# Kernel tuning notes

Measured on AMD Instinct MI355X. Metric: run time of the kernel, lower is better.

Reference implementation:

```python
import jax, jax.numpy as jnp
import numpy as np

B, C, H, W = 32, 4, 512, 512
T = 64  # Angular_representive_Threshold
GROUPS = 2


def setup_inputs() -> dict:
    key = jax.random.key(0)
    k1, k2 = jax.random.split(key)
    x_real = jax.random.normal(k1, (B, C, H, W), dtype=jnp.float32)
    x_imag = jax.random.normal(k2, (B, C, H, W), dtype=jnp.float32)
    return {"x_real": x_real, "x_imag": x_imag}


def reference(x_real, x_imag):
    # Complex angular-delay input, split into 2 groups of 2 channels (torch.chunk dim=1)
    x = (x_real + 1j * x_imag).astype(jnp.complex64)            # [B,4,H,W]
    xg = x.reshape(B, GROUPS, 2, H, W)                          # [B,g,ch,H,W]
    ch0, ch1 = xg[:, :, 0], xg[:, :, 1]                         # [B,g,H,W]
    # sqrt(|real|^2) == |real|; energy difference summed over delay axis H (dim=2)
    diff = (jnp.abs(jnp.abs(ch0.real) - jnp.abs(ch1.imag)) +
            jnp.abs(jnp.abs(ch1.real) - jnp.abs(ch0.imag))).sum(axis=2)  # [B,g,W]
    # torch.sort ascending, keep first T indices (smallest energy difference)
    idx = jnp.argsort(diff, axis=-1)[..., :T]                   # [B,g,T]
    # vectorized column scatter replacing the per-batch/per-threshold python loops
    mask = jnp.zeros((B, GROUPS, W), jnp.float32).at[
        jnp.arange(B)[:, None, None],
        jnp.arange(GROUPS)[None, :, None],
        idx].set(1.0)                                           # [B,g,W]
    xm = xg * mask[:, :, None, None, :]                         # zero non-selected angular bins
    # ifft over delay (dim=-2) then fft over angle (dim=-1), +0.5 on real part
    out = jnp.fft.fft(jnp.fft.ifft(xm, axis=-2), axis=-1) + 0.5
    out = out.reshape(B, C, H, W).astype(jnp.complex64)         # concat of both groups on dim=1
    # return as stacked real/imag float32 (complex64 payload)
    return jnp.stack([out.real, out.imag], axis=-1)             # [B,4,H,W,2]
```

## Files before the change

kernel.cpp:

```cpp
#include <hip/hip_runtime.h>
#include <math.h>

#define NB 32
#define NC 4
#define NH 512
#define NW 512
#define NT 64
#define NG 2
#define BK 32

typedef __attribute__((ext_vector_type(8))) short short8;
typedef __attribute__((ext_vector_type(4))) short short4v;
typedef __attribute__((ext_vector_type(4))) float float4v;

__device__ inline unsigned short f2bf(float f) {
  union { float f; unsigned u; } v; v.f = f;
  unsigned r = v.u + 0x7FFF + ((v.u >> 16) & 1);
  return (unsigned short)(r >> 16);
}

__device__ __forceinline__ void gld16(const unsigned short* g, unsigned short* l) {
  __builtin_amdgcn_global_load_lds(
      (__attribute__((address_space(1))) const unsigned int*)g,
      (__attribute__((address_space(3))) unsigned int*)l, 16, 0, 0);
}

__global__ __launch_bounds__(256) void k_diff(const float* __restrict__ xr,
                                              const float* __restrict__ xi,
                                              float* __restrict__ diffp) {
  int bg = blockIdx.x, hc = blockIdx.y;
  int b = bg >> 1, g = bg & 1;
  size_t c0 = ((size_t)(b * NC + 2 * g)) * NH * NW;
  size_t c1 = c0 + (size_t)NH * NW;
  int t = threadIdx.x;
  int q = t & 127, rg = t >> 7;
  int h0 = hc * 64;
  float4v acc = {0.f, 0.f, 0.f, 0.f};
  for (int r = rg; r < 64; r += 2) {
    size_t o = (size_t)(h0 + r) * NW + q * 4;
    float4v r0 = *(const float4v*)(xr + c0 + o);
    float4v i0 = *(const float4v*)(xi + c0 + o);
    float4v r1 = *(const float4v*)(xr + c1 + o);
    float4v i1 = *(const float4v*)(xi + c1 + o);
#pragma unroll
    for (int k = 0; k < 4; ++k)
      acc[k] += fabsf(fabsf(r0[k]) - fabsf(i1[k])) + fabsf(fabsf(r1[k]) - fabsf(i0[k]));
  }
  __shared__ float4v red[256];
  red[t] = acc;
  __syncthreads();
  if (t < 128) {
    float4v v = red[t];
    float4v u = red[t + 128];
#pragma unroll
    for (int k = 0; k < 4; ++k) v[k] += u[k];
    *(float4v*)(diffp + ((size_t)hc * 64 + bg) * NW + q * 4) = v;
  }
}

__global__ void k_select(const float* __restrict__ diffp, int* __restrict__ sel) {
  __shared__ float v[NW];
  int w = threadIdx.x;
  int bg = blockIdx.x;
  float mine = 0.f;
#pragma unroll
  for (int hc = 0; hc < 8; ++hc) mine += diffp[((size_t)hc * 64 + bg) * NW + w];
  v[w] = mine;
  __syncthreads();
  int rank = 0;
  for (int u = 0; u < NW; ++u) {
    float o = v[u];
    rank += (o < mine) || (o == mine && u < w);
  }
  if (rank < NT) sel[bg * NT + rank] = w;
}

__global__ __launch_bounds__(256) void k_build_T(unsigned short* __restrict__ Tb) {
  __shared__ float2 lt[512];
  int t = threadIdx.x;
  {
    float s, c;
    sincosf(6.2831853071795864769f * (float)t * (1.0f / 512.0f), &s, &c);
    lt[t] = make_float2(c, s);
    sincosf(6.2831853071795864769f * (float)(t + 256) * (1.0f / 512.0f), &s, &c);
    lt[t + 256] = make_float2(c, s);
  }
  __syncthreads();
#pragma unroll
  for (int i = 0; i < 4; ++i) {
    int idx = blockIdx.x * 1024 + i * 256 + t;
    int m = idx >> 10, k = idx & 1023;
    int hm = m & 511, rm = m >> 9;
    int hk = k & 511, rk = k >> 9;
    float2 cs = lt[(hm * hk) & 511];
    float val = (rm == rk) ? cs.x : (rk ? -cs.y : cs.y);
    Tb[idx] = f2bf(val * (1.0f / 512.0f));
  }
}

__global__ __launch_bounds__(256) void k_gather(const float* __restrict__ xr,
                                                const float* __restrict__ xi,
                                                const int* __restrict__ sel,
                                                unsigned short* __restrict__ Xg) {
  __shared__ short jmap[512];
  __shared__ __align__(16) unsigned short tile[2][64][136];
  int img = blockIdx.x, hc = blockIdx.y;
  int t = threadIdx.x;
  int b = img >> 2, g = (img >> 1) & 1;
  jmap[t] = -1;
  jmap[t + 256] = -1;
  __syncthreads();
  if (t < NT) {
    int w = sel[(b * NG + g) * NT + t];
    jmap[w] = (short)t;
  }
  __syncthreads();
  size_t base = (size_t)img * NH * NW + (size_t)hc * 128 * NW;
  for (int i = 0; i < 64; ++i) {
    int lin = i * 256 + t;
    int r = lin >> 7, q = lin & 127;
    size_t o = base + (size_t)r * NW + q * 4;
    float4v vr = *(const float4v*)(xr + o);
    float4v vi = *(const float4v*)(xi + o);
    short4v jm = *(const short4v*)&jmap[q * 4];
#pragma unroll
    for (int k = 0; k < 4; ++k) {
      int j = jm[k];
      if (j >= 0) {
        tile[0][j][r] = f2bf(vr[k]);
        tile[1][j][r] = f2bf(vi[k]);
      }
    }
  }
  __syncthreads();
  int j = t >> 2, s4 = t & 3;
  size_t orow = ((size_t)img * 64 + j) * 1024 + (size_t)hc * 128;
#pragma unroll
  for (int v = 0; v < 4; ++v) {
    int hl = v * 32 + s4 * 8;
    *(short8*)(Xg + orow + hl)       = *(const short8*)&tile[0][j][hl];
    *(short8*)(Xg + orow + 512 + hl) = *(const short8*)&tile[1][j][hl];
  }
}

__global__ __launch_bounds__(256) void k_build_E(const int* __restrict__ sel,
                                                 unsigned short* __restrict__ Eb) {
  __shared__ int wsel[NT];
  __shared__ float2 lt[512];
  int bg = blockIdx.x;
  int t = threadIdx.x;
  {
    float s, c;
    sincosf(6.2831853071795864769f * (float)t * (1.0f / 512.0f), &s, &c);
    lt[t] = make_float2(c, s);
    sincosf(6.2831853071795864769f * (float)(t + 256) * (1.0f / 512.0f), &s, &c);
    lt[t + 256] = make_float2(c, s);
  }
  if (t < NT) wsel[t] = sel[bg * NT + t];
  __syncthreads();
  int base = blockIdx.y * 8192;
#pragma unroll
  for (int i = 0; i < 32; ++i) {
    int idx = base + i * 256 + t;
    int n = idx >> 7, kidx = idx & 127;
    int j = kidx & 63, half = kidx >> 6;
    int part = n >> 9, kk = n & 511;
    int w = wsel[j];
    float2 cs = lt[(kk * w) & 511];
    float val = part == 0 ? (half ? cs.y : cs.x) : (half ? cs.x : -cs.y);
    Eb[(size_t)bg * 131072 + idx] = f2bf(val);
  }
}

__global__ __launch_bounds__(256) void k_gemm3(const unsigned short* __restrict__ Tb,
                                               const unsigned short* __restrict__ Xg,
                                               unsigned short* __restrict__ Yg) {
  __shared__ __align__(16) unsigned short Al[2][128 * BK];
  __shared__ __align__(16) unsigned short Bl[2][128 * BK];
  int lin = blockIdx.y * 64 + blockIdx.x;
  int swz = (lin & 7) * 64 + (lin >> 3);
  int n0 = (swz & 63) * 128;
  int m0 = (swz >> 6) * 128;
  int tid = threadIdx.x;
  int lane = tid & 63, wid = tid >> 6;
  int wm = wid >> 1, wn = wid & 1;
  int quad = lane >> 4, l15 = lane & 15;
  int srow = lane >> 2, sqd = lane & 3;

  float4v acc[4][4];
#pragma unroll
  for (int i = 0; i < 4; ++i)
#pragma unroll
    for (int j = 0; j < 4; ++j) acc[i][j] = (float4v){0.f, 0.f, 0.f, 0.f};

#define STAGE3(buf, kk0)                                                        \
  {                                                                             \
    _Pragma("unroll")                                                           \
    for (int p = 0; p < 2; ++p) {                                               \
      int chunk = wid * 2 + p;                                                  \
      int row = chunk * 16 + srow;                                              \
      int sq = sqd ^ ((row >> 1) & 3);                                          \
      gld16(&Tb[(size_t)(m0 + row) * 1024 + (kk0) + sq * 8], &Al[buf][chunk * 512]); \
      gld16(&Xg[(size_t)(n0 + row) * 1024 + (kk0) + sq * 8], &Bl[buf][chunk * 512]); \
    }                                                                           \
  }

  STAGE3(0, 0);
  __syncthreads();
  int cur = 0;
  for (int t = 0; t < 32; ++t) {
    if (t < 31) STAGE3(cur ^ 1, (t + 1) * 32);

    short8 af[4], bfv[4];
#pragma unroll
    for (int tt = 0; tt < 4; ++tt) {
      int ra = wm * 64 + tt * 16 + l15;
      int rb = wn * 64 + tt * 16 + l15;
      af[tt]  = *(const short8*)&Al[cur][ra * BK + ((quad ^ ((ra >> 1) & 3)) << 3)];
      bfv[tt] = *(const short8*)&Bl[cur][rb * BK + ((quad ^ ((rb >> 1) & 3)) << 3)];
    }
#pragma unroll
    for (int tm = 0; tm < 4; ++tm)
#pragma unroll
      for (int tn = 0; tn < 4; ++tn)
        acc[tm][tn] = __builtin_amdgcn_mfma_f32_16x16x32_bf16(af[tm], bfv[tn], acc[tm][tn], 0, 0, 0);

    __syncthreads();
    cur ^= 1;
  }

#pragma unroll
  for (int tm = 0; tm < 4; ++tm)
#pragma unroll
    for (int tn = 0; tn < 4; ++tn)
#pragma unroll
      for (int r = 0; r < 4; ++r) {
        int m = m0 + wm * 64 + tm * 16 + quad * 4 + r;
        int n = n0 + wn * 64 + tn * 16 + l15;
        int img = n >> 6, j = n & 63;
        int h = m & 511, ri = m >> 9;
        Yg[((size_t)img * 512 + h) * 128 + ri * 64 + j] = f2bf(acc[tm][tn][r]);
      }
}

__global__ __launch_bounds__(256) void k_gemm4(const unsigned short* __restrict__ Yg,
                                               const unsigned short* __restrict__ Eball,
                                               float2* __restrict__ out) {
  __shared__ __align__(16) unsigned short Al[128 * 128];
  __shared__ __align__(16) unsigned short Bl[128 * 128];
  int lin = blockIdx.x + blockIdx.y * 8 + blockIdx.z * 64;
  int swz = (lin & 7) * 512 + (lin >> 3);
  int n0 = (swz & 7) * 64;
  int m0 = ((swz >> 3) & 7) * 128;
  int bg = swz >> 6;
  int b = bg >> 1, g = bg & 1;
  int img0 = b * 4 + 2 * g;
  const unsigned short* Ab = Yg + (size_t)img0 * 512 * 128;
  const unsigned short* Eb = Eball + (size_t)bg * 131072;

  int tid = threadIdx.x;
  int lane = tid & 63, wid = tid >> 6;
  int wm = wid >> 1, wn = wid & 1;
  int quad = lane >> 4, l15 = lane & 15;
  int lrow4 = lane >> 4, cch = lane & 15;

#pragma unroll
  for (int c8 = 0; c8 < 8; ++c8) {
    int call = wid * 8 + c8;
    int row = call * 4 + lrow4;
    int sch = cch ^ (row & 7);
    gld16(&Ab[(size_t)(m0 + row) * 128 + sch * 8], &Al[call * 512]);
    int l = row & 63, wnB = row >> 6;
    int part = l >> 5;
    int grow = part * 512 + n0 + wnB * 32 + (l & 31);
    gld16(&Eb[(size_t)grow * 128 + sch * 8], &Bl[call * 512]);
  }
  __syncthreads();

  float4v acc[4][4];
#pragma unroll
  for (int i = 0; i < 4; ++i)
#pragma unroll
    for (int j = 0; j < 4; ++j) acc[i][j] = (float4v){0.f, 0.f, 0.f, 0.f};

#pragma unroll
  for (int ks = 0; ks < 4; ++ks) {
    short8 af[4], bfv[4];
#pragma unroll
    for (int tt = 0; tt < 4; ++tt) {
      int ra = wm * 64 + tt * 16 + l15;
      int rb = wn * 64 + tt * 16 + l15;
      af[tt]  = *(const short8*)&Al[ra * 128 + (((ks * 4 + quad) ^ (ra & 7)) << 3)];
      bfv[tt] = *(const short8*)&Bl[rb * 128 + (((ks * 4 + quad) ^ (rb & 7)) << 3)];
    }
#pragma unroll
    for (int tm = 0; tm < 4; ++tm)
#pragma unroll
      for (int tn = 0; tn < 4; ++tn)
        acc[tm][tn] = __builtin_amdgcn_mfma_f32_16x16x32_bf16(af[tm], bfv[tn], acc[tm][tn], 0, 0, 0);
  }

#pragma unroll
  for (int tm = 0; tm < 4; ++tm)
#pragma unroll
    for (int t2 = 0; t2 < 2; ++t2)
#pragma unroll
      for (int r = 0; r < 4; ++r) {
        int m = m0 + wm * 64 + tm * 16 + quad * 4 + r;
        int ch = m >> 9, h = m & 511;
        int img = img0 + ch;
        int kk = n0 + wn * 32 + t2 * 16 + l15;
        float2 v = make_float2(acc[tm][t2][r] + 0.5f, acc[tm][t2 + 2][r]);
        out[((size_t)(img * 512 + h)) * 512 + kk] = v;
      }
}

extern "C" void kernel_launch(void* const* d_in, const int* in_sizes, int n_in,
                              void* d_out, int out_size, void* d_ws, size_t ws_size,
                              hipStream_t stream) {
  const float* xr = (const float*)d_in[0];
  const float* xi = (const float*)d_in[1];
  float2* out = (float2*)d_out;

  char* ws = (char*)d_ws;
  float*          diffp = (float*)ws;
  int*            sel   = (int*)(ws + 1048576);
  unsigned short* Tb    = (unsigned short*)(ws + 2097152);
  unsigned short* Xg    = (unsigned short*)(ws + 4194304);
  unsigned short* Yg    = (unsigned short*)(ws + 20971520);
  unsigned short* Eb    = (unsigned short*)(ws + 37748736);

  k_diff   <<<dim3(NB * NG, 8), 256, 0, stream>>>(xr, xi, diffp);
  k_select <<<NB * NG,          NW, 0, stream>>>(diffp, sel);
  k_build_T<<<1024,             256, 0, stream>>>(Tb);
  k_gather <<<dim3(NB * NC, 4), 256, 0, stream>>>(xr, xi, sel, Xg);
  k_build_E<<<dim3(NB * NG, 16),256, 0, stream>>>(sel, Eb);
  k_gemm3  <<<dim3(64, 8),      256, 0, stream>>>(Tb, Xg, Yg);
  k_gemm4  <<<dim3(8, 8, 64),   256, 0, stream>>>(Yg, Eb, out);
}
```

Before: 580.0 us.

## Fuse bf16 transpose into diff pass and gather selected columns inside GEMM

```diff
diff --git a/kernel.cpp b/kernel.cpp
--- a/kernel.cpp
+++ b/kernel.cpp
@@ -10,7 +10,6 @@
 #define BK 32
 
 typedef __attribute__((ext_vector_type(8))) short short8;
-typedef __attribute__((ext_vector_type(4))) short short4v;
 typedef __attribute__((ext_vector_type(4))) float float4v;
 
 __device__ inline unsigned short f2bf(float f) {
@@ -25,27 +24,50 @@
       (__attribute__((address_space(3))) unsigned int*)l, 16, 0, 0);
 }
 
-__global__ __launch_bounds__(256) void k_diff(const float* __restrict__ xr,
-                                              const float* __restrict__ xi,
-                                              float* __restrict__ diffp) {
+__global__ __launch_bounds__(256) void k_diff_t(const float* __restrict__ xr,
+                                                const float* __restrict__ xi,
+                                                float* __restrict__ diffp,
+                                                unsigned short* __restrict__ Xt) {
   int bg = blockIdx.x, hc = blockIdx.y;
   int b = bg >> 1, g = bg & 1;
-  size_t c0 = ((size_t)(b * NC + 2 * g)) * NH * NW;
-  size_t c1 = c0 + (size_t)NH * NW;
+  int c0 = b * NC + 2 * g, c1 = c0 + 1;
   int t = threadIdx.x;
   int q = t & 127, rg = t >> 7;
-  int h0 = hc * 64;
+  int h0 = hc * 64 + rg * 32;
   float4v acc = {0.f, 0.f, 0.f, 0.f};
-  for (int r = rg; r < 64; r += 2) {
-    size_t o = (size_t)(h0 + r) * NW + q * 4;
-    float4v r0 = *(const float4v*)(xr + c0 + o);
-    float4v i0 = *(const float4v*)(xi + c0 + o);
-    float4v r1 = *(const float4v*)(xr + c1 + o);
-    float4v i1 = *(const float4v*)(xi + c1 + o);
-#pragma unroll
-    for (int k = 0; k < 4; ++k)
-      acc[k] += fabsf(fabsf(r0[k]) - fabsf(i1[k])) + fabsf(fabsf(r1[k]) - fabsf(i0[k]));
-  }
+
+#pragma unroll
+  for (int phase = 0; phase < 2; ++phase) {
+    const float* PA = (phase ? xr + (size_t)c1 * NH * NW : xr + (size_t)c0 * NH * NW);
+    const float* PB = (phase ? xi + (size_t)c0 * NH * NW : xi + (size_t)c1 * NH * NW);
+    int icA = phase ? c1 : c0;
+    int icB = phase ? c0 : c1;
+    size_t colA = (size_t)h0;
+    size_t colB = (size_t)512 + h0;
+#pragma unroll
+    for (int i8 = 0; i8 < 4; ++i8) {
+      short8 bA[4], bB[4];
+#pragma unroll
+      for (int u = 0; u < 8; ++u) {
+        int h = h0 + i8 * 8 + u;
+        float4v a  = *(const float4v*)(PA + (size_t)h * NW + q * 4);
+        float4v bb = *(const float4v*)(PB + (size_t)h * NW + q * 4);
+#pragma unroll
+        for (int k = 0; k < 4; ++k) {
+          acc[k] += fabsf(fabsf(a[k]) - fabsf(bb[k]));
+          bA[k][u] = (short)f2bf(a[k]);
+          bB[k][u] = (short)f2bf(bb[k]);
+        }
+      }
+#pragma unroll
+      for (int k = 0; k < 4; ++k) {
+        int w = q * 4 + k;
+        *(short8*)(Xt + ((size_t)(icA * 512 + w)) * 1024 + colA + i8 * 8) = bA[k];
+        *(short8*)(Xt + ((size_t)(icB * 512 + w)) * 1024 + colB + i8 * 8) = bB[k];
+      }
+    }
+  }
+
   __shared__ float4v red[256];
   red[t] = acc;
   __syncthreads();
@@ -86,61 +108,19 @@
     lt[t + 256] = make_float2(c, s);
   }
   __syncthreads();
-#pragma unroll
-  for (int i = 0; i < 4; ++i) {
-    int idx = blockIdx.x * 1024 + i * 256 + t;
-    int m = idx >> 10, k = idx & 1023;
-    int hm = m & 511, rm = m >> 9;
-    int hk = k & 511, rk = k >> 9;
+  int idx0 = (blockIdx.x * 256 + t) * 8;
+  int m = idx0 >> 10, k0 = idx0 & 1023;
+  int hm = m & 511, rm = m >> 9;
+  int rk = k0 >> 9;
+  short8 o;
+#pragma unroll
+  for (int u = 0; u < 8; ++u) {
+    int hk = (k0 + u) & 511;
     float2 cs = lt[(hm * hk) & 511];
     float val = (rm == rk) ? cs.x : (rk ? -cs.y : cs.y);
-    Tb[idx] = f2bf(val * (1.0f / 512.0f));
-  }
-}
-
-__global__ __launch_bounds__(256) void k_gather(const float* __restrict__ xr,
-                                                const float* __restrict__ xi,
-                                                const int* __restrict__ sel,
-                                                unsigned short* __restrict__ Xg) {
-  __shared__ short jmap[512];
-  __shared__ __align__(16) unsigned short tile[2][64][136];
-  int img = blockIdx.x, hc = blockIdx.y;
-  int t = threadIdx.x;
-  int b = img >> 2, g = (img >> 1) & 1;
-  jmap[t] = -1;
-  jmap[t + 256] = -1;
-  __syncthreads();
-  if (t < NT) {
-    int w = sel[(b * NG + g) * NT + t];
-    jmap[w] = (short)t;
-  }
-  __syncthreads();
-  size_t base = (size_t)img * NH * NW + (size_t)hc * 128 * NW;
-  for (int i = 0; i < 64; ++i) {
-    int lin = i * 256 + t;
-    int r = lin >> 7, q = lin & 127;
-    size_t o = base + (size_t)r * NW + q * 4;
-    float4v vr = *(const float4v*)(xr + o);
-    float4v vi = *(const float4v*)(xi + o);
-    short4v jm = *(const short4v*)&jmap[q * 4];
-#pragma unroll
-    for (int k = 0; k < 4; ++k) {
-      int j = jm[k];
-      if (j >= 0) {
-        tile[0][j][r] = f2bf(vr[k]);
-        tile[1][j][r] = f2bf(vi[k]);
-      }
-    }
-  }
-  __syncthreads();
-  int j = t >> 2, s4 = t & 3;
-  size_t orow = ((size_t)img * 64 + j) * 1024 + (size_t)hc * 128;
-#pragma unroll
-  for (int v = 0; v < 4; ++v) {
-    int hl = v * 32 + s4 * 8;
-    *(short8*)(Xg + orow + hl)       = *(const short8*)&tile[0][j][hl];
-    *(short8*)(Xg + orow + 512 + hl) = *(const short8*)&tile[1][j][hl];
-  }
+    o[u] = (short)f2bf(val * (1.0f / 512.0f));
+  }
+  *(short8*)(Tb + idx0) = o;
 }
 
 __global__ __launch_bounds__(256) void k_build_E(const int* __restrict__ sel,
@@ -160,20 +140,26 @@
   __syncthreads();
   int base = blockIdx.y * 8192;
 #pragma unroll
-  for (int i = 0; i < 32; ++i) {
-    int idx = base + i * 256 + t;
-    int n = idx >> 7, kidx = idx & 127;
-    int j = kidx & 63, half = kidx >> 6;
+  for (int i = 0; i < 4; ++i) {
+    int idx0 = base + (i * 256 + t) * 8;
+    int n = idx0 >> 7, kidx0 = idx0 & 127;
+    int j0 = kidx0 & 63, half = kidx0 >> 6;
     int part = n >> 9, kk = n & 511;
-    int w = wsel[j];
-    float2 cs = lt[(kk * w) & 511];
-    float val = part == 0 ? (half ? cs.y : cs.x) : (half ? cs.x : -cs.y);
-    Eb[(size_t)bg * 131072 + idx] = f2bf(val);
+    short8 o;
+#pragma unroll
+    for (int u = 0; u < 8; ++u) {
+      int w = wsel[j0 + u];
+      float2 cs = lt[(kk * w) & 511];
+      float val = part == 0 ? (half ? cs.y : cs.x) : (half ? cs.x : -cs.y);
+      o[u] = (short)f2bf(val);
+    }
+    *(short8*)(Eb + (size_t)bg * 131072 + idx0) = o;
   }
 }
 
 __global__ __launch_bounds__(256) void k_gemm3(const unsigned short* __restrict__ Tb,
-                                               const unsigned short* __restrict__ Xg,
+                                               const unsigned short* __restrict__ Xt,
+                                               const int* __restrict__ sel,
                                                unsigned short* __restrict__ Yg) {
   __shared__ __align__(16) unsigned short Al[2][128 * BK];
   __shared__ __align__(16) unsigned short Bl[2][128 * BK];
@@ -181,28 +167,41 @@
   int swz = (lin & 7) * 64 + (lin >> 3);
   int n0 = (swz & 63) * 128;
   int m0 = (swz >> 6) * 128;
+  int img0 = n0 >> 6;
+  int bg = (img0 >> 2) * 2 + ((img0 >> 1) & 1);
   int tid = threadIdx.x;
   int lane = tid & 63, wid = tid >> 6;
   int wm = wid >> 1, wn = wid & 1;
   int quad = lane >> 4, l15 = lane & 15;
   int srow = lane >> 2, sqd = lane & 3;
 
+  const unsigned short* srcA[2];
+  const unsigned short* srcB[2];
+#pragma unroll
+  for (int p = 0; p < 2; ++p) {
+    int chunk = wid * 2 + p;
+    int row = chunk * 16 + srow;
+    int sq = sqd ^ ((row >> 1) & 3);
+    srcA[p] = Tb + (size_t)(m0 + row) * 1024 + sq * 8;
+    int imgB = img0 + (row >> 6), j = row & 63;
+    int w = sel[bg * NT + j];
+    srcB[p] = Xt + ((size_t)(imgB * 512 + w)) * 1024 + sq * 8;
+  }
+
   float4v acc[4][4];
 #pragma unroll
   for (int i = 0; i < 4; ++i)
 #pragma unroll
     for (int j = 0; j < 4; ++j) acc[i][j] = (float4v){0.f, 0.f, 0.f, 0.f};
 
-#define STAGE3(buf, kk0)                                                        \
-  {                                                                             \
-    _Pragma("unroll")                                                           \
-    for (int p = 0; p < 2; ++p) {                                               \
-      int chunk = wid * 2 + p;                                                  \
-      int row = chunk * 16 + srow;                                              \
-      int sq = sqd ^ ((row >> 1) & 3);                                          \
-      gld16(&Tb[(size_t)(m0 + row) * 1024 + (kk0) + sq * 8], &Al[buf][chunk * 512]); \
-      gld16(&Xg[(size_t)(n0 + row) * 1024 + (kk0) + sq * 8], &Bl[buf][chunk * 512]); \
-    }                                                                           \
+#define STAGE3(buf, kk0)                                          \
+  {                                                               \
+    _Pragma("unroll")                                             \
+    for (int p = 0; p < 2; ++p) {                                 \
+      int chunk = wid * 2 + p;                                    \
+      gld16(srcA[p] + (kk0), &Al[buf][chunk * 512]);              \
+      gld16(srcB[p] + (kk0), &Bl[buf][chunk * 512]);              \
+    }                                                             \
   }
 
   STAGE3(0, 0);
@@ -326,15 +325,14 @@
   float*          diffp = (float*)ws;
   int*            sel   = (int*)(ws + 1048576);
   unsigned short* Tb    = (unsigned short*)(ws + 2097152);
-  unsigned short* Xg    = (unsigned short*)(ws + 4194304);
+  unsigned short* Eb    = (unsigned short*)(ws + 4194304);
   unsigned short* Yg    = (unsigned short*)(ws + 20971520);
-  unsigned short* Eb    = (unsigned short*)(ws + 37748736);
-
-  k_diff   <<<dim3(NB * NG, 8), 256, 0, stream>>>(xr, xi, diffp);
+  unsigned short* Xt    = (unsigned short*)(ws + 37748736);
+
+  k_diff_t <<<dim3(NB * NG, 8), 256, 0, stream>>>(xr, xi, diffp, Xt);
   k_select <<<NB * NG,          NW, 0, stream>>>(diffp, sel);
-  k_build_T<<<1024,             256, 0, stream>>>(Tb);
-  k_gather <<<dim3(NB * NC, 4), 256, 0, stream>>>(xr, xi, sel, Xg);
+  k_build_T<<<512,              256, 0, stream>>>(Tb);
   k_build_E<<<dim3(NB * NG, 16),256, 0, stream>>>(sel, Eb);
-  k_gemm3  <<<dim3(64, 8),      256, 0, stream>>>(Tb, Xg, Yg);
+  k_gemm3  <<<dim3(64, 8),      256, 0, stream>>>(Tb, Xt, sel, Yg);
   k_gemm4  <<<dim3(8, 8, 64),   256, 0, stream>>>(Yg, Eb, out);
 }
```

New measurement: 646.8 us. 1.12x slower.
